# Kernel tuning notes

Hardware: AMD Instinct MI355X
Metric: run time of the kernel (lower is better)

The kernel has to match this reference:

```python
import jax, jax.numpy as jnp
import numpy as np

BS, S, D, H, HS, HSEL, L = 32, 512, 512, 8, 2, 4, 6
DK = D // H  # 64
HD = H - HS  # dynamic heads


def setup_inputs() -> dict:
    key = jax.random.key(0)
    ks = jax.random.split(key, 10)
    w = lambda k, shape: jax.random.normal(k, shape, dtype=jnp.float32) * 0.02
    return {
        'q_embed_data': jax.random.normal(ks[0], (BS, S, D), jnp.float32),
        'qa_embed_data': jax.random.normal(ks[1], (BS, S, D), jnp.float32),
        # stacked per-layer params (torch Linear convention: W[out,in], y = x@W.T+b)
        'Wq': w(ks[2], (L, D, D)), 'bq': jnp.zeros((L, D), jnp.float32),
        'Wv': w(ks[3], (L, D, D)), 'bv': jnp.zeros((L, D), jnp.float32),
        'Wg': w(ks[4], (L, HD, D)),                      # routing gate, no bias
        'Wo': w(ks[5], (L, D, D)), 'bo': jnp.zeros((L, D), jnp.float32),
        'ln1_g': jnp.ones((L, D), jnp.float32), 'ln1_b': jnp.zeros((L, D), jnp.float32),
        'W1': w(ks[6], (L, D, D)), 'b1': jnp.zeros((L, D), jnp.float32),
        'W2': w(ks[7], (L, D, D)), 'b2': jnp.zeros((L, D), jnp.float32),
        'ln2_g': jnp.ones((L, D), jnp.float32), 'ln2_b': jnp.zeros((L, D), jnp.float32),
    }


def _layer_norm(x, g, b):
    m = x.mean(-1, keepdims=True)
    v = ((x - m) ** 2).mean(-1, keepdims=True)
    return (x - m) * jax.lax.rsqrt(v + 1e-5) * g + b


def _moh_attention(xq, xv, Wq, bq, Wv, bv, Wg, Wo, bo, strict):
    bs, s, d = xq.shape
    q = xq @ Wq.T + bq            # kq_same=True: k = q projection
    v = xv @ Wv.T + bv
    qh = q.reshape(bs, s, H, DK).transpose(0, 2, 1, 3)   # [b,h,s,dk]
    vh = v.reshape(bs, s, H, DK).transpose(0, 2, 1, 3)
    scores = jnp.einsum('bhqd,bhkd->bhqk', qh, qh) / jnp.sqrt(jnp.float32(DK))
    # mask==1 -> causal incl. diag; mask==0 -> strictly causal
    allow = jnp.tril(jnp.ones((s, s), bool), k=-1 if strict else 0)
    scores = jnp.where(allow, scores, jnp.float32(-1e9))
    # pad-zero shift: first query row replaced by zeros -> uniform attention
    scores = scores.at[:, :, 0, :].set(0.0)
    # per-token top-k head routing over dynamic heads
    gates = jax.nn.softmax(q.reshape(bs * s, D) @ Wg.T, axis=-1)  # [bs*s, HD]
    _, idx = jax.lax.top_k(gates, HSEL)
    dmask = jnp.zeros_like(gates).at[jnp.arange(bs * s)[:, None], idx].set(1.0)
    dyn = (gates * dmask).reshape(bs, s, HD)
    routing = jnp.concatenate([jnp.ones((bs, s, HS), gates.dtype), dyn], -1).mean(1)  # [b,H]
    attn = jax.nn.softmax(scores, axis=-1)
    ctx = jnp.einsum('bhqk,bhkd->bhqd', attn, vh) * routing[:, :, None, None]
    out = ctx.transpose(0, 2, 1, 3).reshape(bs, s, D) @ Wo.T + bo
    f = dmask.sum(0)
    P = gates.mean(0)
    balance = jnp.sum((f / (f.sum() + 1e-5)) * (P / (P.sum() + 1e-5)))
    return out, balance


def reference(q_embed_data, qa_embed_data, Wq, bq, Wv, bv, Wg, Wo, bo,
              ln1_g, ln1_b, W1, b1, W2, b2, ln2_g, ln2_b):
    def layer(i, xq, xv, strict):
        a, bl = _moh_attention(xq, xv, Wq[i], bq[i], Wv[i], bv[i], Wg[i], Wo[i], bo[i], strict)
        x = _layer_norm(xq + a, ln1_g[i], ln1_b[i])
        ffn = jax.nn.relu(x @ W1[i].T + b1[i]) @ W2[i].T + b2[i]
        return _layer_norm(x + ffn, ln2_g[i], ln2_b[i]), bl

    y = qa_embed_data
    x = q_embed_data
    # blocks_1: self-attention on y, mask=1
    y, _ = layer(0, y, y, False)
    y, _ = layer(1, y, y, False)
    # blocks_2: alternate mask=1 self-attn / mask=0 cross-attn (values=y)
    x, _ = layer(2, x, x, False)
    x, bl = layer(3, x, y, True)
    x, _ = layer(4, x, x, False)
    x, bl = layer(5, x, y, True)
    return (x, bl)
```

## Files before the change

### kernel.cpp

```cpp
#include <hip/hip_runtime.h>
#include <cstdint>

#define BSZ 32
#define SEQ 512
#define DM  512
#define NH  8
#define DK  64
#define HS_ 2
#define HD_ 6
#define NL  6
#define MROWS (BSZ*SEQ)
#define QVLD 1024
#define SCL 0.18033688011112043f

typedef unsigned short bf16_t;
typedef __attribute__((ext_vector_type(4))) float f32x4;
typedef __attribute__((ext_vector_type(8))) short bf16x8;
typedef __attribute__((ext_vector_type(8))) unsigned short u16x8;

#define DEV static __device__ __forceinline__

DEV float bf2f(bf16_t b) {
  unsigned int u = ((unsigned int)b) << 16;
  float f; __builtin_memcpy(&f, &u, 4); return f;
}
DEV bf16_t f2b(float f) {
  unsigned int u; __builtin_memcpy(&u, &f, 4);
  unsigned int r = (u + 0x7fffu + ((u >> 16) & 1u)) >> 16;
  return (bf16_t)r;
}
DEV void unp2(unsigned int w, float& a, float& b) {
  unsigned int ua = w << 16, ub = w & 0xffff0000u;
  __builtin_memcpy(&a, &ua, 4); __builtin_memcpy(&b, &ub, 4);
}
DEV unsigned cvtpk(float lo, float hi) {
  unsigned r;
  asm("v_cvt_pk_bf16_f32 %0, %1, %2" : "=v"(r) : "v"(lo), "v"(hi));
  return r;
}

DEV void gload_lds16(const bf16_t* g, bf16_t* l) {
  __builtin_amdgcn_global_load_lds(
      (const __attribute__((address_space(1))) void*)g,
      (__attribute__((address_space(3))) void*)l, 16, 0, 0);
}

__global__ __launch_bounds__(256) void f2b2_kernel(
    const float* __restrict__ s0, const float* __restrict__ s1,
    bf16_t* __restrict__ d0, bf16_t* __restrict__ d1) {
  const float* s = blockIdx.y ? s1 : s0;
  bf16_t* d = blockIdx.y ? d1 : d0;
  const int i = blockIdx.x * 256 + threadIdx.x;
  float4 v = reinterpret_cast<const float4*>(s)[i];
  ushort4 o;
  o.x = f2b(v.x); o.y = f2b(v.y); o.z = f2b(v.z); o.w = f2b(v.w);
  reinterpret_cast<ushort4*>(d)[i] = o;
}

__global__ __launch_bounds__(256) void f2bw_kernel(
    const float* __restrict__ s0, const float* __restrict__ s1,
    const float* __restrict__ s2, const float* __restrict__ s3,
    const float* __restrict__ s4, bf16_t* __restrict__ dst) {
  const float* srcs[5] = {s0, s1, s2, s3, s4};
  const float* s = srcs[blockIdx.y];
  bf16_t* d = dst + (size_t)blockIdx.y * ((size_t)NL * DM * DM);
  const int i = blockIdx.x * 256 + threadIdx.x;
  float4 v = reinterpret_cast<const float4*>(s)[i];
  ushort4 o;
  o.x = f2b(v.x); o.y = f2b(v.y); o.z = f2b(v.z); o.w = f2b(v.w);
  reinterpret_cast<ushort4*>(d)[i] = o;
}

__global__ __launch_bounds__(256) void gemm_qv(
    const bf16_t* __restrict__ A0, const bf16_t* __restrict__ A1,
    const bf16_t* __restrict__ W0, const bf16_t* __restrict__ W1,
    const float* __restrict__ b0, const float* __restrict__ b1,
    bf16_t* __restrict__ Yb) {
  const int K = 512;
  const int lin = blockIdx.y * 8 + blockIdx.x;
  const int swz = (lin & 7) * 128 + (lin >> 3);
  const int bn = swz & 7, bm = swz >> 3;
  const int tid = threadIdx.x, wid = tid >> 6, lane = tid & 63;
  const int wr = wid >> 1, wc = wid & 1;
  __shared__ __align__(16) bf16_t As[128 * 64];
  __shared__ __align__(16) bf16_t Bs[128 * 64];

  const bool hi = bn >= 4;
  const bf16_t* Asel = hi ? A1 : A0;
  const bf16_t* Wsel = hi ? (W1 - (size_t)512 * K) : W0;
  const float* bsel = hi ? (b1 - 512) : b0;

  f32x4 acc[4][4];
#pragma unroll
  for (int m = 0; m < 4; ++m)
#pragma unroll
    for (int n = 0; n < 4; ++n) acc[m][n] = f32x4{0.f, 0.f, 0.f, 0.f};

  const int lrow = lane & 15, lko = (lane >> 4) * 8;
  const int sr = wid * 8 + (lane >> 3), scol = (lane & 7) * 8;
  const size_t arow0 = (size_t)bm * 128, brow0 = (size_t)bn * 128;

  for (int k0 = 0; k0 < K; k0 += 64) {
#pragma unroll
    for (int i = 0; i < 4; ++i) {
      gload_lds16(Asel + (arow0 + i * 32 + sr) * K + k0 + scol, &As[(i * 4 + wid) * 512]);
      gload_lds16(Wsel + (brow0 + i * 32 + sr) * K + k0 + scol, &Bs[(i * 4 + wid) * 512]);
    }
    __syncthreads();
    bf16x8 af[4][2], bw[4][2];
#pragma unroll
    for (int m = 0; m < 4; ++m)
#pragma unroll
      for (int ks = 0; ks < 2; ++ks)
        af[m][ks] = *reinterpret_cast<const bf16x8*>(
            &As[(wr * 64 + m * 16 + lrow) * 64 + ks * 32 + lko]);
#pragma unroll
    for (int n = 0; n < 4; ++n)
#pragma unroll
      for (int ks = 0; ks < 2; ++ks)
        bw[n][ks] = *reinterpret_cast<const bf16x8*>(
            &Bs[(wc * 64 + n * 16 + lrow) * 64 + ks * 32 + lko]);
    __builtin_amdgcn_s_setprio(1);
#pragma unroll
    for (int ks = 0; ks < 2; ++ks)
#pragma unroll
      for (int m = 0; m < 4; ++m)
#pragma unroll
        for (int n = 0; n < 4; ++n)
          acc[m][n] = __builtin_amdgcn_mfma_f32_16x16x32_bf16(af[m][ks], bw[n][ks], acc[m][n], 0, 0, 0);
    __builtin_amdgcn_s_setprio(0);
    __syncthreads();
  }

  const int r0 = bm * 128 + wr * 64 + (lane >> 4) * 4;
  const int c0 = bn * 128 + wc * 64 + lrow;
#pragma unroll
  for (int n = 0; n < 4; ++n) {
    const int col = c0 + n * 16;
    const float bc = bsel[col];
#pragma unroll
    for (int m = 0; m < 4; ++m)
#pragma unroll
      for (int j = 0; j < 4; ++j)
        Yb[(size_t)(r0 + m * 16 + j) * QVLD + col] = f2b(acc[m][n][j] + bc);
  }
}

template <bool RELU>
__global__ __launch_bounds__(256) void gemm_n512(
    const bf16_t* __restrict__ A, const bf16_t* __restrict__ W,
    const float* __restrict__ bias, bf16_t* __restrict__ Yb) {
  const int K = 512;
  const int lin = blockIdx.y * 4 + blockIdx.x;
  const int swz = (lin & 7) * 128 + (lin >> 3);
  const int bn = swz & 3, bm = swz >> 2;
  const int tid = threadIdx.x, wid = tid >> 6, lane = tid & 63;
  const int wr = wid >> 1, wc = wid & 1;
  __shared__ __align__(16) bf16_t As[64 * 64];
  __shared__ __align__(16) bf16_t Bs[128 * 64];

  f32x4 acc[2][4];
#pragma unroll
  for (int m = 0; m < 2; ++m)
#pragma unroll
    for (int n = 0; n < 4; ++n) acc[m][n] = f32x4{0.f, 0.f, 0.f, 0.f};

  const int lrow = lane & 15, lko = (lane >> 4) * 8;
  const int sr = wid * 8 + (lane >> 3), scol = (lane & 7) * 8;
  const size_t arow0 = (size_t)bm * 64, brow0 = (size_t)bn * 128;

  for (int k0 = 0; k0 < K; k0 += 64) {
#pragma unroll
    for (int i = 0; i < 2; ++i)
      gload_lds16(A + (arow0 + i * 32 + sr) * K + k0 + scol, &As[(i * 4 + wid) * 512]);
#pragma unroll
    for (int i = 0; i < 4; ++i)
      gload_lds16(W + (brow0 + i * 32 + sr) * K + k0 + scol, &Bs[(i * 4 + wid) * 512]);
    __syncthreads();
    bf16x8 af[2][2], bw[4][2];
#pragma unroll
    for (int m = 0; m < 2; ++m)
#pragma unroll
      for (int ks = 0; ks < 2; ++ks)
        af[m][ks] = *reinterpret_cast<const bf16x8*>(
            &As[(wr * 32 + m * 16 + lrow) * 64 + ks * 32 + lko]);
#pragma unroll
    for (int n = 0; n < 4; ++n)
#pragma unroll
      for (int ks = 0; ks < 2; ++ks)
        bw[n][ks] = *reinterpret_cast<const bf16x8*>(
            &Bs[(wc * 64 + n * 16 + lrow) * 64 + ks * 32 + lko]);
    __builtin_amdgcn_s_setprio(1);
#pragma unroll
    for (int ks = 0; ks < 2; ++ks)
#pragma unroll
      for (int m = 0; m < 2; ++m)
#pragma unroll
        for (int n = 0; n < 4; ++n)
          acc[m][n] = __builtin_amdgcn_mfma_f32_16x16x32_bf16(af[m][ks], bw[n][ks], acc[m][n], 0, 0, 0);
    __builtin_amdgcn_s_setprio(0);
    __syncthreads();
  }

  const int r0 = bm * 64 + wr * 32 + (lane >> 4) * 4;
  const int c0 = bn * 128 + wc * 64 + lrow;
#pragma unroll
  for (int n = 0; n < 4; ++n) {
    const int col = c0 + n * 16;
    const float bc = bias[col];
#pragma unroll
    for (int m = 0; m < 2; ++m)
#pragma unroll
      for (int j = 0; j < 4; ++j) {
        float v = acc[m][n][j] + bc;
        if (RELU) v = fmaxf(v, 0.f);
        Yb[(size_t)(r0 + m * 16 + j) * DM + col] = f2b(v);
      }
  }
}

__global__ __launch_bounds__(256) void gates_kernel(
    const bf16_t* __restrict__ qv, const float* __restrict__ Wg,
    float* __restrict__ rdyn, float* __restrict__ fP) {
  __shared__ float wg_s[HD_ * DM];
  __shared__ float blk[4][18];
  const int tid = threadIdx.x, wid = tid >> 6, lane = tid & 63;
  for (int i = tid; i < HD_ * DM / 4; i += 256)
    reinterpret_cast<float4*>(wg_s)[i] = reinterpret_cast<const float4*>(Wg)[i];
  __syncthreads();
  const int bb = blockIdx.x >> 3;
  const int t0 = (blockIdx.x & 7) * 64 + wid * 16;
  float fs[6] = {0, 0, 0, 0, 0, 0}, ps[6] = {0, 0, 0, 0, 0, 0}, rs[6] = {0, 0, 0, 0, 0, 0};
  for (int it = 0; it < 16; ++it) {
    const int tok = bb * SEQ + t0 + it;
    uint4 u = reinterpret_cast<const uint4*>(qv + (size_t)tok * QVLD)[lane];
    float x[8];
    unp2(u.x, x[0], x[1]); unp2(u.y, x[2], x[3]);
    unp2(u.z, x[4], x[5]); unp2(u.w, x[6], x[7]);
    float g[6];
#pragma unroll
    for (int j = 0; j < 6; ++j) {
      float p = 0.f;
#pragma unroll
      for (int e = 0; e < 8; ++e) p = fmaf(x[e], wg_s[j * DM + lane * 8 + e], p);
#pragma unroll
      for (int off = 32; off; off >>= 1) p += __shfl_xor(p, off);
      g[j] = p;
    }
    float mx = g[0];
#pragma unroll
    for (int j = 1; j < 6; ++j) mx = fmaxf(mx, g[j]);
    float se = 0.f;
#pragma unroll
    for (int j = 0; j < 6; ++j) { g[j] = __expf(g[j] - mx); se += g[j]; }
    float inv = 1.f / se;
#pragma unroll
    for (int j = 0; j < 6; ++j) g[j] *= inv;
    int d1 = 0;
#pragma unroll
    for (int j = 1; j < 6; ++j)
      if (g[j] < g[d1] || (g[j] == g[d1] && j > d1)) d1 = j;
    int d2 = (d1 == 0) ? 1 : 0;
#pragma unroll
    for (int j = 0; j < 6; ++j) {
      if (j == d1) continue;
      if (g[j] < g[d2] || (g[j] == g[d2] && j > d2)) d2 = j;
    }
#pragma unroll
    for (int j = 0; j < 6; ++j) {
      const bool drop = (j == d1) || (j == d2);
      fs[j] += drop ? 0.f : 1.f;
      ps[j] += g[j];
      rs[j] += drop ? 0.f : g[j];
    }
  }
  if (lane == 0) {
#pragma unroll
    for (int j = 0; j < 6; ++j) {
      blk[wid][j] = fs[j]; blk[wid][6 + j] = ps[j]; blk[wid][12 + j] = rs[j];
    }
  }
  __syncthreads();
  if (tid < 18) {
    float s = blk[0][tid] + blk[1][tid] + blk[2][tid] + blk[3][tid];
    if (tid < 12) atomicAdd(&fP[tid], s);
    else atomicAdd(&rdyn[bb * 6 + (tid - 12)], s * (1.f / 512.f));
  }
}

__global__ __launch_bounds__(256, 2) void fattn_kernel(
    const bf16_t* __restrict__ qv, const float* __restrict__ rdyn,
    bf16_t* __restrict__ ctx, int strict) {
  const int lin = (blockIdx.z * 8 + blockIdx.y) * 2 + blockIdx.x;
  const int swz = (lin & 7) * 64 + (lin >> 3);
  const int bx = swz & 1, h = (swz >> 1) & 7, b = swz >> 4;
  const int tid = threadIdx.x, wid = tid >> 6, lane = tid & 63;
  const int c0 = lane & 15, grp = lane >> 4;
  const int l3 = lane >> 3, c3 = lane & 7;
  const int kidx = lane & 31, dhalf = lane >> 5;

  __shared__ __align__(16) bf16_t Ks[2][64 * 64];
  __shared__ __align__(16) bf16_t Vt[2][64 * 72];
  __shared__ __align__(16) bf16_t Ps[4][32 * 64];
  __shared__ float csum[64];

  const bf16_t* qp = qv;
  const bf16_t* vp = qv + 512;
  const float factor = (h < HS_) ? 1.f : rdyn[b * 6 + (h - HS_)];

  const int qtA = bx, qtB = 3 - bx;
  const int qbaseA = qtA * 128 + wid * 32;
  const int qbaseB = qtB * 128 + wid * 32;

  bf16x8 qfA[2][2], qfB[2][2];
#pragma unroll
  for (int nt = 0; nt < 2; ++nt)
#pragma unroll
    for (int ks = 0; ks < 2; ++ks) {
      qfA[nt][ks] = *reinterpret_cast<const bf16x8*>(
          qp + ((size_t)(b * SEQ + qbaseA + nt * 16 + c0)) * QVLD + h * DK + ks * 32 + grp * 8);
      qfB[nt][ks] = *reinterpret_cast<const bf16x8*>(
          qp + ((size_t)(b * SEQ + qbaseB + nt * 16 + c0)) * QVLD + h * DK + ks * 32 + grp * 8);
    }

  f32x4 accA[2][4], accB[2][4];
#pragma unroll
  for (int m = 0; m < 2; ++m)
#pragma unroll
    for (int d = 0; d < 4; ++d) {
      accA[m][d] = f32x4{0.f, 0.f, 0.f, 0.f};
      accB[m][d] = f32x4{0.f, 0.f, 0.f, 0.f};
    }
  float mA[2] = {-3e38f, -3e38f}, lA[2] = {0.f, 0.f};
  float mB[2] = {-3e38f, -3e38f}, lB[2] = {0.f, 0.f};
  float cs[8] = {0, 0, 0, 0, 0, 0, 0, 0};

  const int lastA = (qbaseA + 31 - strict) >> 6;
  const int lastB = (qbaseB + 31 - strict) >> 6;
  const int ktmax = 2 * qtB + 1;

  auto stageK = [&](int kt, bf16_t* dst) {
#pragma unroll
    for (int i = 0; i < 2; ++i) {
      int row = i * 32 + wid * 8 + l3;
      int blk = c3 ^ l3;
      gload_lds16(qp + ((size_t)(b * SEQ + kt * 64 + row)) * QVLD + h * DK + blk * 8,
                  dst + (i * 32 + wid * 8) * 64);
    }
  };
  auto loadV = [&](int kt, ushort4 (&lo)[2], ushort4 (&hv)[2]) {
#pragma unroll
    for (int j = 0; j < 2; ++j) {
      const int d0 = (wid * 2 + j) * 8 + dhalf * 4;
      const bf16_t* src = vp + ((size_t)(b * SEQ + kt * 64 + 2 * kidx)) * QVLD + h * DK + d0;
      lo[j] = *reinterpret_cast<const ushort4*>(src);
      hv[j] = *reinterpret_cast<const ushort4*>(src + QVLD);
    }
  };
  auto writeV = [&](bf16_t* Vtb, ushort4 (&lo)[2], ushort4 (&hv)[2]) {
#pragma unroll
    for (int j = 0; j < 2; ++j) {
      const int d0 = (wid * 2 + j) * 8 + dhalf * 4;
      *reinterpret_cast<unsigned*>(&Vtb[(d0 + 0) * 72 + 2 * kidx]) = (unsigned)lo[j].x | ((unsigned)hv[j].x << 16);
      *reinterpret_cast<unsigned*>(&Vtb[(d0 + 1) * 72 + 2 * kidx]) = (unsigned)lo[j].y | ((unsigned)hv[j].y << 16);
      *reinterpret_cast<unsigned*>(&Vtb[(d0 + 2) * 72 + 2 * kidx]) = (unsigned)lo[j].z | ((unsigned)hv[j].z << 16);
      *reinterpret_cast<unsigned*>(&Vtb[(d0 + 3) * 72 + 2 * kidx]) = (unsigned)lo[j].w | ((unsigned)hv[j].w << 16);
      if (bx == 0) {
        cs[j * 4 + 0] += bf2f(lo[j].x) + bf2f(hv[j].x);
        cs[j * 4 + 1] += bf2f(lo[j].y) + bf2f(hv[j].y);
        cs[j * 4 + 2] += bf2f(lo[j].z) + bf2f(hv[j].z);
        cs[j * 4 + 3] += bf2f(lo[j].w) + bf2f(hv[j].w);
      }
    }
  };

  auto do_tile = [&](bf16x8 (&qf)[2][2], f32x4 (&acc)[2][4], float (&mreg)[2],
                     float (&lreg)[2], int qbase, bool masked, int kt,
                     const bf16_t* Ksb, const bf16_t* Vtb) {
    const char* KsB = (const char*)Ksb;
    bf16x8 kf[4][2];
#pragma unroll
    for (int mt = 0; mt < 4; ++mt)
#pragma unroll
      for (int ks = 0; ks < 2; ++ks)
        kf[mt][ks] = *reinterpret_cast<const bf16x8*>(
            KsB + (mt * 16 + c0) * 128 + 16 * ((4 * ks + grp) ^ (c0 & 7)));
    f32x4 s[4][2];
#pragma unroll
    for (int mt = 0; mt < 4; ++mt)
#pragma unroll
      for (int nt = 0; nt < 2; ++nt) s[mt][nt] = f32x4{0.f, 0.f, 0.f, 0.f};
    __builtin_amdgcn_s_setprio(1);
#pragma unroll
    for (int mt = 0; mt < 4; ++mt)
#pragma unroll
      for (int nt = 0; nt < 2; ++nt)
#pragma unroll
        for (int ks = 0; ks < 2; ++ks)
          s[mt][nt] = __builtin_amdgcn_mfma_f32_16x16x32_bf16(
              kf[mt][ks], qf[nt][ks], s[mt][nt], 0, 0, 0);
    __builtin_amdgcn_s_setprio(0);

    float sc[2];
#pragma unroll
    for (int nt = 0; nt < 2; ++nt) {
      const int q = qbase + nt * 16 + c0;
#pragma unroll
      for (int mt = 0; mt < 4; ++mt)
#pragma unroll
        for (int j = 0; j < 4; ++j) {
          int k = kt * 64 + mt * 16 + grp * 4 + j;
          float t = s[mt][nt][j] * SCL;
          if (masked && (k + strict > q)) t = -1e30f;
          s[mt][nt][j] = t;
        }
      float mx = -3e38f;
#pragma unroll
      for (int mt = 0; mt < 4; ++mt)
#pragma unroll
        for (int j = 0; j < 4; ++j) mx = fmaxf(mx, s[mt][nt][j]);
      mx = fmaxf(mx, __shfl_xor(mx, 16));
      mx = fmaxf(mx, __shfl_xor(mx, 32));
      const float mnew = fmaxf(mreg[nt], mx);
      sc[nt] = exp2f(mreg[nt] - mnew);
      mreg[nt] = mnew;
      float ts = 0.f;
#pragma unroll
      for (int mt = 0; mt < 4; ++mt)
#pragma unroll
        for (int j = 0; j < 4; ++j) {
          float pp = exp2f(s[mt][nt][j] - mnew);
          s[mt][nt][j] = pp; ts += pp;
        }
      ts += __shfl_xor(ts, 16);
      ts += __shfl_xor(ts, 32);
      lreg[nt] = lreg[nt] * sc[nt] + ts;
    }
    char* PsB = (char*)(&Ps[wid][0]);
#pragma unroll
    for (int nt = 0; nt < 2; ++nt)
#pragma unroll
      for (int mt = 0; mt < 4; ++mt) {
        uint2 w;
        w.x = cvtpk(s[mt][nt][0], s[mt][nt][1]);
        w.y = cvtpk(s[mt][nt][2], s[mt][nt][3]);
        int row = nt * 16 + c0;
        int off = (row * 128 + mt * 32 + grp * 8) ^ ((c0 & 7) << 4);
        *reinterpret_cast<uint2*>(PsB + off) = w;
      }
#pragma unroll
    for (int mtq = 0; mtq < 2; ++mtq) {
      f32x4 sv;
#pragma unroll
      for (int j = 0; j < 4; ++j) sv[j] = __shfl(sc[mtq], grp * 4 + j);
#pragma unroll
      for (int dt = 0; dt < 4; ++dt) acc[mtq][dt] *= sv;
    }
    bf16x8 pf[2][2], vf2[4][2];
#pragma unroll
    for (int mtq = 0; mtq < 2; ++mtq)
#pragma unroll
      for (int ks = 0; ks < 2; ++ks)
        pf[mtq][ks] = *reinterpret_cast<const bf16x8*>(
            PsB + (mtq * 16 + c0) * 128 + 16 * ((4 * ks + grp) ^ (c0 & 7)));
#pragma unroll
    for (int dt = 0; dt < 4; ++dt)
#pragma unroll
      for (int ks = 0; ks < 2; ++ks)
        vf2[dt][ks] = *reinterpret_cast<const bf16x8*>(
            (const char*)Vtb + (dt * 16 + c0) * 144 + ks * 64 + grp * 16);
    __builtin_amdgcn_s_setprio(1);
#pragma unroll
    for (int mtq = 0; mtq < 2; ++mtq)
#pragma unroll
      for (int dt = 0; dt < 4; ++dt)
#pragma unroll
        for (int ks = 0; ks < 2; ++ks)
          acc[mtq][dt] = __builtin_amdgcn_mfma_f32_16x16x32_bf16(
              pf[mtq][ks], vf2[dt][ks], acc[mtq][dt], 0, 0, 0);
    __builtin_amdgcn_s_setprio(0);
  };

  {
    ushort4 lo[2], hv[2];
    stageK(0, Ks[0]);
    loadV(0, lo, hv);
    writeV(Vt[0], lo, hv);
    __syncthreads();
  }

  int cbuf = 0;
  for (int kt = 0; kt <= ktmax; ++kt, cbuf ^= 1) {
    ushort4 lo[2], hv[2];
    const bool pref = kt < ktmax;
    if (pref) {
      stageK(kt + 1, Ks[cbuf ^ 1]);
      loadV(kt + 1, lo, hv);
    }
    if (kt <= lastB) do_tile(qfB, accB, mB, lB, qbaseB, kt == lastB, kt, Ks[cbuf], Vt[cbuf]);
    if (kt <= lastA) do_tile(qfA, accA, mA, lA, qbaseA, kt == lastA, kt, Ks[cbuf], Vt[cbuf]);
    if (pref) writeV(Vt[cbuf ^ 1], lo, hv);
    __syncthreads();
  }

  if (bx == 0) {
#pragma unroll
    for (int e = 0; e < 8; ++e)
#pragma unroll
      for (int off = 1; off <= 16; off <<= 1) cs[e] += __shfl_xor(cs[e], off);
    if ((lane & 31) == 0) {
#pragma unroll
      for (int e = 0; e < 8; ++e)
        csum[(wid * 2 + (e >> 2)) * 8 + dhalf * 4 + (e & 3)] = cs[e];
    }
  }
  __syncthreads();
  if (bx == 0 && tid < 64)
    ctx[((size_t)(b * SEQ)) * DM + h * DK + tid] = f2b(csum[tid] * (1.f / 512.f) * factor);

#pragma unroll
  for (int e = 0; e < 2; ++e) {
    const int qbase = e ? qbaseB : qbaseA;
    f32x4 (&acc)[2][4] = e ? accB : accA;
    float (&lreg)[2] = e ? lB : lA;
#pragma unroll
    for (int mtq = 0; mtq < 2; ++mtq) {
      const float inv = factor / lreg[mtq];
      f32x4 iv;
#pragma unroll
      for (int j = 0; j < 4; ++j) iv[j] = __shfl(inv, grp * 4 + j);
#pragma unroll
      for (int j = 0; j < 4; ++j) {
        const int q = qbase + mtq * 16 + grp * 4 + j;
        if (q == 0) continue;
#pragma unroll
        for (int dt = 0; dt < 4; ++dt)
          ctx[((size_t)(b * SEQ + q)) * DM + h * DK + dt * 16 + c0] =
              f2b(acc[mtq][dt][j] * iv[j]);
      }
    }
  }
}

template <int OUT>
__global__ __launch_bounds__(256) void add_ln_kernel(
    const bf16_t* __restrict__ X, const bf16_t* __restrict__ A2,
    const float* __restrict__ gam, const float* __restrict__ bet,
    bf16_t* __restrict__ outb, float* __restrict__ outf) {
  const int wid = threadIdx.x >> 6, lane = threadIdx.x & 63;
  const size_t row = (size_t)blockIdx.x * 4 + wid;
  const size_t base = row * DM + lane * 8;
  uint4 xu = *reinterpret_cast<const uint4*>(X + base);
  uint4 au = *reinterpret_cast<const uint4*>(A2 + base);
  float z[8];
  {
    float p0, p1, q0, q1;
    unp2(xu.x, p0, p1); unp2(au.x, q0, q1); z[0] = p0 + q0; z[1] = p1 + q1;
    unp2(xu.y, p0, p1); unp2(au.y, q0, q1); z[2] = p0 + q0; z[3] = p1 + q1;
    unp2(xu.z, p0, p1); unp2(au.z, q0, q1); z[4] = p0 + q0; z[5] = p1 + q1;
    unp2(xu.w, p0, p1); unp2(au.w, q0, q1); z[6] = p0 + q0; z[7] = p1 + q1;
  }
  float s = 0.f;
#pragma unroll
  for (int e = 0; e < 8; ++e) s += z[e];
#pragma unroll
  for (int off = 32; off; off >>= 1) s += __shfl_xor(s, off);
  const float mean = s * (1.f / 512.f);
  float ss = 0.f;
#pragma unroll
  for (int e = 0; e < 8; ++e) { float d = z[e] - mean; ss += d * d; }
#pragma unroll
  for (int off = 32; off; off >>= 1) ss += __shfl_xor(ss, off);
  const float inv = rsqrtf(ss * (1.f / 512.f) + 1e-5f);
  float4 g0 = *reinterpret_cast<const float4*>(gam + lane * 8);
  float4 g1 = *reinterpret_cast<const float4*>(gam + lane * 8 + 4);
  float4 b0 = *reinterpret_cast<const float4*>(bet + lane * 8);
  float4 b1 = *reinterpret_cast<const float4*>(bet + lane * 8 + 4);
  float o[8];
  o[0] = (z[0] - mean) * inv * g0.x + b0.x;
  o[1] = (z[1] - mean) * inv * g0.y + b0.y;
  o[2] = (z[2] - mean) * inv * g0.z + b0.z;
  o[3] = (z[3] - mean) * inv * g0.w + b0.w;
  o[4] = (z[4] - mean) * inv * g1.x + b1.x;
  o[5] = (z[5] - mean) * inv * g1.y + b1.y;
  o[6] = (z[6] - mean) * inv * g1.z + b1.z;
  o[7] = (z[7] - mean) * inv * g1.w + b1.w;
  if (OUT == 0) {
    uint4 w;
    w.x = (unsigned)f2b(o[0]) | ((unsigned)f2b(o[1]) << 16);
    w.y = (unsigned)f2b(o[2]) | ((unsigned)f2b(o[3]) << 16);
    w.z = (unsigned)f2b(o[4]) | ((unsigned)f2b(o[5]) << 16);
    w.w = (unsigned)f2b(o[6]) | ((unsigned)f2b(o[7]) << 16);
    *reinterpret_cast<uint4*>(outb + base) = w;
  } else {
    float4 f0, f1;
    f0.x = o[0]; f0.y = o[1]; f0.z = o[2]; f0.w = o[3];
    f1.x = o[4]; f1.y = o[5]; f1.z = o[6]; f1.w = o[7];
    *reinterpret_cast<float4*>(outf + base) = f0;
    *reinterpret_cast<float4*>(outf + base + 4) = f1;
  }
}

__global__ void balance_kernel(const float* __restrict__ fP, float* __restrict__ out) {
  if (threadIdx.x == 0 && blockIdx.x == 0) {
    float fs = 0.f, pssum = 0.f, P[6];
    for (int j = 0; j < 6; ++j) {
      fs += fP[j];
      P[j] = fP[6 + j] * (1.f / (float)MROWS);
      pssum += P[j];
    }
    float bal = 0.f;
    for (int j = 0; j < 6; ++j)
      bal += (fP[j] / (fs + 1e-5f)) * (P[j] / (pssum + 1e-5f));
    out[0] = bal;
  }
}

extern "C" void kernel_launch(void* const* d_in, const int* in_sizes, int n_in,
                              void* d_out, int out_size, void* d_ws, size_t ws_size,
                              hipStream_t stream) {
  (void)in_sizes; (void)n_in; (void)out_size; (void)ws_size;
  const float* q_embed  = (const float*)d_in[0];
  const float* qa_embed = (const float*)d_in[1];
  const float* Wq  = (const float*)d_in[2];
  const float* bq  = (const float*)d_in[3];
  const float* Wv  = (const float*)d_in[4];
  const float* bv  = (const float*)d_in[5];
  const float* Wg  = (const float*)d_in[6];
  const float* Wo  = (const float*)d_in[7];
  const float* bo  = (const float*)d_in[8];
  const float* ln1g = (const float*)d_in[9];
  const float* ln1b = (const float*)d_in[10];
  const float* W1  = (const float*)d_in[11];
  const float* b1  = (const float*)d_in[12];
  const float* W2  = (const float*)d_in[13];
  const float* b2  = (const float*)d_in[14];
  const float* ln2g = (const float*)d_in[15];
  const float* ln2b = (const float*)d_in[16];

  char* p = (char*)d_ws;
  auto alloc = [&](size_t bytes) -> char* {
    char* r = p; p += (bytes + 255) & ~(size_t)255; return r;
  };
  const size_t WDE = (size_t)NL * DM * DM;
  const size_t AE  = (size_t)MROWS * DM;
  bf16_t* wall_b = (bf16_t*)alloc(5 * WDE * 2);
  bf16_t* wq_b = wall_b;
  bf16_t* wv_b = wall_b + WDE;
  bf16_t* wo_b = wall_b + 2 * WDE;
  bf16_t* w1_b = wall_b + 3 * WDE;
  bf16_t* w2_b = wall_b + 4 * WDE;
  bf16_t* y_b   = (bf16_t*)alloc(AE * 2);
  bf16_t* x_b   = (bf16_t*)alloc(AE * 2);
  bf16_t* qv_b  = (bf16_t*)alloc((size_t)MROWS * QVLD * 2);
  bf16_t* ctx_b = (bf16_t*)alloc(AE * 2);
  bf16_t* x1_b  = (bf16_t*)alloc(AE * 2);
  bf16_t* tmp_b = (bf16_t*)alloc(AE * 2);
  bf16_t* ffn1_b = (bf16_t*)alloc(AE * 2);
  float* stats = (float*)alloc(NL * (12 + BSZ * 6) * 4);
  float* fPbase = stats;
  float* rdynbase = stats + NL * 12;

  hipMemsetAsync(stats, 0, NL * (12 + BSZ * 6) * 4, stream);

  f2bw_kernel<<<dim3((unsigned)(WDE / 4 / 256), 5), 256, 0, stream>>>(
      Wq, Wv, Wo, W1, W2, wall_b);
  f2b2_kernel<<<dim3((unsigned)(AE / 4 / 256), 2), 256, 0, stream>>>(
      qa_embed, q_embed, y_b, x_b);

  const size_t DD = (size_t)DM * DM;
  dim3 gqv(8, 128), gn5(4, 256);
  float* outx = (float*)d_out;

  auto layer = [&](int i, bf16_t* resb, const bf16_t* xvb, int strict, bool last) {
    float* fP = fPbase + i * 12;
    float* rdyn = rdynbase + i * (BSZ * 6);
    gemm_qv<<<gqv, 256, 0, stream>>>(
        resb, xvb, wq_b + i * DD, wv_b + i * DD, bq + i * DM, bv + i * DM, qv_b);
    gates_kernel<<<MROWS / 64, 256, 0, stream>>>(qv_b, Wg + (size_t)i * HD_ * DM, rdyn, fP);
    fattn_kernel<<<dim3(2, NH, BSZ), 256, 0, stream>>>(qv_b, rdyn, ctx_b, strict);
    gemm_n512<false><<<gn5, 256, 0, stream>>>(ctx_b, wo_b + i * DD, bo + i * DM, tmp_b);
    add_ln_kernel<0><<<MROWS / 4, 256, 0, stream>>>(
        resb, tmp_b, ln1g + i * DM, ln1b + i * DM, x1_b, nullptr);
    gemm_n512<true><<<gn5, 256, 0, stream>>>(x1_b, w1_b + i * DD, b1 + i * DM, ffn1_b);
    gemm_n512<false><<<gn5, 256, 0, stream>>>(ffn1_b, w2_b + i * DD, b2 + i * DM, tmp_b);
    if (last)
      add_ln_kernel<1><<<MROWS / 4, 256, 0, stream>>>(
          x1_b, tmp_b, ln2g + i * DM, ln2b + i * DM, nullptr, outx);
    else
      add_ln_kernel<0><<<MROWS / 4, 256, 0, stream>>>(
          x1_b, tmp_b, ln2g + i * DM, ln2b + i * DM, resb, nullptr);
  };

  layer(0, y_b, y_b, 0, false);
  layer(1, y_b, y_b, 0, false);
  layer(2, x_b, x_b, 0, false);
  layer(3, x_b, y_b, 1, false);
  layer(4, x_b, x_b, 0, false);
  layer(5, x_b, y_b, 1, true);
  balance_kernel<<<1, 64, 0, stream>>>(fPbase + 5 * 12, outx + (size_t)MROWS * DM);
}
```

Measured before the change: 1.024 ms.

## Single-buffer K/V tiles, fold softmax scale into Q, defer rescaling

The flash-attention kernel now folds the exp2 softmax scale into the Q fragments once at load time instead of scaling every score. It skips the running-max update and accumulator rescale when the new tile max exceeds the old one by at most 8 (a lazy-rescale threshold), which saves exp2 calls and accumulator multiplies. It also drops K/V double buffering in favour of single-buffered load, sync, compute, sync. That halves the K/V LDS footprint but stops the next tile's loads from overlapping the current tile's compute, and rounding Q after scaling adds a little bf16 error.

```diff
diff --git a/kernel.cpp b/kernel.cpp
--- a/kernel.cpp
+++ b/kernel.cpp
@@ -43,6 +43,18 @@
   __builtin_amdgcn_global_load_lds(
       (const __attribute__((address_space(1))) void*)g,
       (__attribute__((address_space(3))) void*)l, 16, 0, 0);
+}
+
+DEV bf16x8 scale_q(bf16x8 v) {
+  u16x8 u;
+  __builtin_memcpy(&u, &v, 16);
+  unsigned w[4];
+#pragma unroll
+  for (int e = 0; e < 4; ++e)
+    w[e] = cvtpk(bf2f(u[2 * e]) * SCL, bf2f(u[2 * e + 1]) * SCL);
+  bf16x8 r;
+  __builtin_memcpy(&r, w, 16);
+  return r;
 }
 
 __global__ __launch_bounds__(256) void f2b2_kernel(
@@ -299,8 +311,8 @@
   const int l3 = lane >> 3, c3 = lane & 7;
   const int kidx = lane & 31, dhalf = lane >> 5;
 
-  __shared__ __align__(16) bf16_t Ks[2][64 * 64];
-  __shared__ __align__(16) bf16_t Vt[2][64 * 72];
+  __shared__ __align__(16) bf16_t Ks[64 * 64];
+  __shared__ __align__(16) bf16_t Vt[64 * 72];
   __shared__ __align__(16) bf16_t Ps[4][32 * 64];
   __shared__ float csum[64];
 
@@ -317,10 +329,10 @@
   for (int nt = 0; nt < 2; ++nt)
 #pragma unroll
     for (int ks = 0; ks < 2; ++ks) {
-      qfA[nt][ks] = *reinterpret_cast<const bf16x8*>(
-          qp + ((size_t)(b * SEQ + qbaseA + nt * 16 + c0)) * QVLD + h * DK + ks * 32 + grp * 8);
-      qfB[nt][ks] = *reinterpret_cast<const bf16x8*>(
-          qp + ((size_t)(b * SEQ + qbaseB + nt * 16 + c0)) * QVLD + h * DK + ks * 32 + grp * 8);
+      qfA[nt][ks] = scale_q(*reinterpret_cast<const bf16x8*>(
+          qp + ((size_t)(b * SEQ + qbaseA + nt * 16 + c0)) * QVLD + h * DK + ks * 32 + grp * 8));
+      qfB[nt][ks] = scale_q(*reinterpret_cast<const bf16x8*>(
+          qp + ((size_t)(b * SEQ + qbaseB + nt * 16 + c0)) * QVLD + h * DK + ks * 32 + grp * 8));
     }
 
   f32x4 accA[2][4], accB[2][4];
@@ -339,45 +351,9 @@
   const int lastB = (qbaseB + 31 - strict) >> 6;
   const int ktmax = 2 * qtB + 1;
 
-  auto stageK = [&](int kt, bf16_t* dst) {
-#pragma unroll
-    for (int i = 0; i < 2; ++i) {
-      int row = i * 32 + wid * 8 + l3;
-      int blk = c3 ^ l3;
-      gload_lds16(qp + ((size_t)(b * SEQ + kt * 64 + row)) * QVLD + h * DK + blk * 8,
-                  dst + (i * 32 + wid * 8) * 64);
-    }
-  };
-  auto loadV = [&](int kt, ushort4 (&lo)[2], ushort4 (&hv)[2]) {
-#pragma unroll
-    for (int j = 0; j < 2; ++j) {
-      const int d0 = (wid * 2 + j) * 8 + dhalf * 4;
-      const bf16_t* src = vp + ((size_t)(b * SEQ + kt * 64 + 2 * kidx)) * QVLD + h * DK + d0;
-      lo[j] = *reinterpret_cast<const ushort4*>(src);
-      hv[j] = *reinterpret_cast<const ushort4*>(src + QVLD);
-    }
-  };
-  auto writeV = [&](bf16_t* Vtb, ushort4 (&lo)[2], ushort4 (&hv)[2]) {
-#pragma unroll
-    for (int j = 0; j < 2; ++j) {
-      const int d0 = (wid * 2 + j) * 8 + dhalf * 4;
-      *reinterpret_cast<unsigned*>(&Vtb[(d0 + 0) * 72 + 2 * kidx]) = (unsigned)lo[j].x | ((unsigned)hv[j].x << 16);
-      *reinterpret_cast<unsigned*>(&Vtb[(d0 + 1) * 72 + 2 * kidx]) = (unsigned)lo[j].y | ((unsigned)hv[j].y << 16);
-      *reinterpret_cast<unsigned*>(&Vtb[(d0 + 2) * 72 + 2 * kidx]) = (unsigned)lo[j].z | ((unsigned)hv[j].z << 16);
-      *reinterpret_cast<unsigned*>(&Vtb[(d0 + 3) * 72 + 2 * kidx]) = (unsigned)lo[j].w | ((unsigned)hv[j].w << 16);
-      if (bx == 0) {
-        cs[j * 4 + 0] += bf2f(lo[j].x) + bf2f(hv[j].x);
-        cs[j * 4 + 1] += bf2f(lo[j].y) + bf2f(hv[j].y);
-        cs[j * 4 + 2] += bf2f(lo[j].z) + bf2f(hv[j].z);
-        cs[j * 4 + 3] += bf2f(lo[j].w) + bf2f(hv[j].w);
-      }
-    }
-  };
-
   auto do_tile = [&](bf16x8 (&qf)[2][2], f32x4 (&acc)[2][4], float (&mreg)[2],
-                     float (&lreg)[2], int qbase, bool masked, int kt,
-                     const bf16_t* Ksb, const bf16_t* Vtb) {
-    const char* KsB = (const char*)Ksb;
+                     float (&lreg)[2], int qbase, bool masked, int kt) {
+    const char* KsB = (const char*)Ks;
     bf16x8 kf[4][2];
 #pragma unroll
     for (int mt = 0; mt < 4; ++mt)
@@ -401,29 +377,40 @@
               kf[mt][ks], qf[nt][ks], s[mt][nt], 0, 0, 0);
     __builtin_amdgcn_s_setprio(0);
 
+    if (masked) {
+#pragma unroll
+      for (int nt = 0; nt < 2; ++nt) {
+        const int q = qbase + nt * 16 + c0;
+#pragma unroll
+        for (int mt = 0; mt < 4; ++mt)
+#pragma unroll
+          for (int j = 0; j < 4; ++j) {
+            int k = kt * 64 + mt * 16 + grp * 4 + j;
+            if (k + strict > q) s[mt][nt][j] = -1e30f;
+          }
+      }
+    }
+    float mx[2];
+#pragma unroll
+    for (int nt = 0; nt < 2; ++nt) {
+      float a = fmaxf(s[0][nt][0], s[0][nt][1]);
+      a = fmaxf(fmaxf(a, s[0][nt][2]), s[0][nt][3]);
+      float bm_ = fmaxf(s[1][nt][0], s[1][nt][1]);
+      bm_ = fmaxf(fmaxf(bm_, s[1][nt][2]), s[1][nt][3]);
+      float c = fmaxf(s[2][nt][0], s[2][nt][1]);
+      c = fmaxf(fmaxf(c, s[2][nt][2]), s[2][nt][3]);
+      float d = fmaxf(s[3][nt][0], s[3][nt][1]);
+      d = fmaxf(fmaxf(d, s[3][nt][2]), s[3][nt][3]);
+      float m_ = fmaxf(fmaxf(a, bm_), fmaxf(c, d));
+      m_ = fmaxf(m_, __shfl_xor(m_, 16));
+      m_ = fmaxf(m_, __shfl_xor(m_, 32));
+      mx[nt] = m_;
+    }
+    const bool defer = __all((mx[0] - mreg[0] <= 8.f) && (mx[1] - mreg[1] <= 8.f));
     float sc[2];
 #pragma unroll
     for (int nt = 0; nt < 2; ++nt) {
-      const int q = qbase + nt * 16 + c0;
-#pragma unroll
-      for (int mt = 0; mt < 4; ++mt)
-#pragma unroll
-        for (int j = 0; j < 4; ++j) {
-          int k = kt * 64 + mt * 16 + grp * 4 + j;
-          float t = s[mt][nt][j] * SCL;
-          if (masked && (k + strict > q)) t = -1e30f;
-          s[mt][nt][j] = t;
-        }
-      float mx = -3e38f;
-#pragma unroll
-      for (int mt = 0; mt < 4; ++mt)
-#pragma unroll
-        for (int j = 0; j < 4; ++j) mx = fmaxf(mx, s[mt][nt][j]);
-      mx = fmaxf(mx, __shfl_xor(mx, 16));
-      mx = fmaxf(mx, __shfl_xor(mx, 32));
-      const float mnew = fmaxf(mreg[nt], mx);
-      sc[nt] = exp2f(mreg[nt] - mnew);
-      mreg[nt] = mnew;
+      const float mnew = defer ? mreg[nt] : fmaxf(mreg[nt], mx[nt]);
       float ts = 0.f;
 #pragma unroll
       for (int mt = 0; mt < 4; ++mt)
@@ -434,7 +421,13 @@
         }
       ts += __shfl_xor(ts, 16);
       ts += __shfl_xor(ts, 32);
-      lreg[nt] = lreg[nt] * sc[nt] + ts;
+      if (defer) {
+        lreg[nt] += ts;
+      } else {
+        sc[nt] = exp2f(mreg[nt] - mnew);
+        lreg[nt] = lreg[nt] * sc[nt] + ts;
+        mreg[nt] = mnew;
+      }
     }
     char* PsB = (char*)(&Ps[wid][0]);
 #pragma unroll
@@ -448,13 +441,15 @@
         int off = (row * 128 + mt * 32 + grp * 8) ^ ((c0 & 7) << 4);
         *reinterpret_cast<uint2*>(PsB + off) = w;
       }
-#pragma unroll
-    for (int mtq = 0; mtq < 2; ++mtq) {
-      f32x4 sv;
-#pragma unroll
-      for (int j = 0; j < 4; ++j) sv[j] = __shfl(sc[mtq], grp * 4 + j);
-#pragma unroll
-      for (int dt = 0; dt < 4; ++dt) acc[mtq][dt] *= sv;
+    if (!defer) {
+#pragma unroll
+      for (int mtq = 0; mtq < 2; ++mtq) {
+        f32x4 sv;
+#pragma unroll
+        for (int j = 0; j < 4; ++j) sv[j] = __shfl(sc[mtq], grp * 4 + j);
+#pragma unroll
+        for (int dt = 0; dt < 4; ++dt) acc[mtq][dt] *= sv;
+      }
     }
     bf16x8 pf[2][2], vf2[4][2];
 #pragma unroll
@@ -468,7 +463,7 @@
 #pragma unroll
       for (int ks = 0; ks < 2; ++ks)
         vf2[dt][ks] = *reinterpret_cast<const bf16x8*>(
-            (const char*)Vtb + (dt * 16 + c0) * 144 + ks * 64 + grp * 16);
+            (const char*)Vt + (dt * 16 + c0) * 144 + ks * 64 + grp * 16);
     __builtin_amdgcn_s_setprio(1);
 #pragma unroll
     for (int mtq = 0; mtq < 2; ++mtq)
@@ -481,25 +476,34 @@
     __builtin_amdgcn_s_setprio(0);
   };
 
-  {
-    ushort4 lo[2], hv[2];
-    stageK(0, Ks[0]);
-    loadV(0, lo, hv);
-    writeV(Vt[0], lo, hv);
+  for (int kt = 0; kt <= ktmax; ++kt) {
+#pragma unroll
+    for (int i = 0; i < 2; ++i) {
+      int row = i * 32 + wid * 8 + l3;
+      int blk = c3 ^ l3;
+      gload_lds16(qp + ((size_t)(b * SEQ + kt * 64 + row)) * QVLD + h * DK + blk * 8,
+                  Ks + (i * 32 + wid * 8) * 64);
+    }
+#pragma unroll
+    for (int j = 0; j < 2; ++j) {
+      const int d0 = (wid * 2 + j) * 8 + dhalf * 4;
+      const bf16_t* src = vp + ((size_t)(b * SEQ + kt * 64 + 2 * kidx)) * QVLD + h * DK + d0;
+      ushort4 lo = *reinterpret_cast<const ushort4*>(src);
+      ushort4 hv = *reinterpret_cast<const ushort4*>(src + QVLD);
+      *reinterpret_cast<unsigned*>(&Vt[(d0 + 0) * 72 + 2 * kidx]) = (unsigned)lo.x | ((unsigned)hv.x << 16);
+      *reinterpret_cast<unsigned*>(&Vt[(d0 + 1) * 72 + 2 * kidx]) = (unsigned)lo.y | ((unsigned)hv.y << 16);
+      *reinterpret_cast<unsigned*>(&Vt[(d0 + 2) * 72 + 2 * kidx]) = (unsigned)lo.z | ((unsigned)hv.z << 16);
+      *reinterpret_cast<unsigned*>(&Vt[(d0 + 3) * 72 + 2 * kidx]) = (unsigned)lo.w | ((unsigned)hv.w << 16);
+      if (bx == 0) {
+        cs[j * 4 + 0] += bf2f(lo.x) + bf2f(hv.x);
+        cs[j * 4 + 1] += bf2f(lo.y) + bf2f(hv.y);
+        cs[j * 4 + 2] += bf2f(lo.z) + bf2f(hv.z);
+        cs[j * 4 + 3] += bf2f(lo.w) + bf2f(hv.w);
+      }
+    }
     __syncthreads();
-  }
-
-  int cbuf = 0;
-  for (int kt = 0; kt <= ktmax; ++kt, cbuf ^= 1) {
-    ushort4 lo[2], hv[2];
-    const bool pref = kt < ktmax;
-    if (pref) {
-      stageK(kt + 1, Ks[cbuf ^ 1]);
-      loadV(kt + 1, lo, hv);
-    }
-    if (kt <= lastB) do_tile(qfB, accB, mB, lB, qbaseB, kt == lastB, kt, Ks[cbuf], Vt[cbuf]);
-    if (kt <= lastA) do_tile(qfA, accA, mA, lA, qbaseA, kt == lastA, kt, Ks[cbuf], Vt[cbuf]);
-    if (pref) writeV(Vt[cbuf ^ 1], lo, hv);
+    if (kt <= lastB) do_tile(qfB, accB, mB, lB, qbaseB, kt == lastB, kt);
+    if (kt <= lastA) do_tile(qfA, accA, mA, lA, qbaseA, kt == lastA, kt);
     __syncthreads();
   }
 
```

Measured after the change: 1.013 ms. No clear change (-1.1%).
